# Optimization experiments

Measured on AMD Instinct MI355X. Metric: run time of the kernel, lower is better.

## Reference

```python
import jax, jax.numpy as jnp
import numpy as np

HIDDEN = 1024


def setup_inputs() -> dict:
    key = jax.random.key(0)
    ks = jax.random.split(key, 8)
    x_in, y_in, out_dim, hidden = 1024, 1024, 1024, HIDDEN
    Nx, Ny = 4096, 4096
    s = lambda d: 1.0 / np.sqrt(d)
    return {
        "x": jax.random.normal(ks[0], (Nx, x_in), jnp.float32),
        "y": jax.random.normal(ks[1], (Ny, y_in), jnp.float32),
        "Wq": jax.random.normal(ks[2], (hidden, x_in), jnp.float32) * s(x_in),
        "bq": jnp.zeros((hidden,), jnp.float32),
        "Wk": jax.random.normal(ks[3], (hidden, y_in), jnp.float32) * s(y_in),
        "bk": jnp.zeros((hidden,), jnp.float32),
        "Wv": jax.random.normal(ks[4], (out_dim, y_in), jnp.float32) * s(y_in),
        "bv": jnp.zeros((out_dim,), jnp.float32),
    }


def reference(x, y, Wq, bq, Wk, bk, Wv, bv):
    # Linear projections (torch Linear: x @ W.T + b)
    q = x @ Wq.T + bq          # [Nx, H]
    k = y @ Wk.T + bk          # [Ny, H]
    v = y @ Wv.T + bv          # [Ny, D_out]
    scores = (q @ k.T) / jnp.sqrt(jnp.asarray(HIDDEN, q.dtype))  # [Nx, Ny]
    attn = jax.nn.softmax(scores, axis=1)
    return attn @ v            # [Nx, D_out]
```

## Files before the change

kernel.cpp:

```cpp
#include <hip/hip_runtime.h>
#include <cstdint>
#include <cstddef>

typedef __attribute__((ext_vector_type(8))) __bf16 bf16x8;
typedef __attribute__((ext_vector_type(4))) float  f32x4;

#define WAITCNT_VM(n)   ((n & 0xF) | 0x70 | 0xF00 | (((n) >> 4) << 14))
#define WAITCNT_LGKM(n) (0xF | 0x70 | ((n) << 8) | (3 << 14))

__device__ __forceinline__ unsigned short f32_to_bf16(float f) {
    union { float f; unsigned int u; } cv;
    cv.f = f;
    unsigned int u = cv.u;
    return (unsigned short)((u + 0x7fffu + ((u >> 16) & 1u)) >> 16);
}

__device__ __forceinline__ float bf16_to_f32(unsigned short h) {
    union { unsigned int u; float f; } cv;
    cv.u = ((unsigned int)h) << 16;
    return cv.f;
}

__device__ __forceinline__ void async_copy16(const unsigned short* g, unsigned short* lds) {
    __builtin_amdgcn_global_load_lds(
        (const __attribute__((address_space(1))) unsigned int*)g,
        (__attribute__((address_space(3))) unsigned int*)lds,
        16, 0, 0);
}

__global__ __launch_bounds__(256) void cast_all(
    const float* __restrict__ x,  const float* __restrict__ y,
    const float* __restrict__ wq, const float* __restrict__ wk, const float* __restrict__ wv,
    unsigned short* __restrict__ xb,  unsigned short* __restrict__ yb,
    unsigned short* __restrict__ wqb, unsigned short* __restrict__ wkb,
    unsigned short* __restrict__ wvb, float* __restrict__ lsum)
{
    int b = blockIdx.x;
    if (b >= 11264) {
        float4 z = {0.f, 0.f, 0.f, 0.f};
#pragma unroll
        for (int t = 0; t < 4; ++t)
            ((float4*)lsum)[threadIdx.x * 4 + t] = z;
        return;
    }
    const float* s; unsigned short* d; int base;
    if      (b < 4096)  { s = x;  d = xb;  base = b; }
    else if (b < 8192)  { s = y;  d = yb;  base = b - 4096; }
    else if (b < 9216)  { s = wq; d = wqb; base = b - 8192; }
    else if (b < 10240) { s = wk; d = wkb; base = b - 9216; }
    else                { s = wv; d = wvb; base = b - 10240; }
    int i = base * 256 + threadIdx.x;
    float4 v = ((const float4*)s)[i];
    ushort4 o;
    o.x = f32_to_bf16(v.x);
    o.y = f32_to_bf16(v.y);
    o.z = f32_to_bf16(v.z);
    o.w = f32_to_bf16(v.w);
    ((ushort4*)d)[i] = o;
}

__device__ __forceinline__ void gemm_core_pf(
    const unsigned short* __restrict__ A, const unsigned short* __restrict__ B,
    int K, int rowBase, int colBase, int kBeg, int kEnd,
    unsigned short* ldsA, unsigned short* ldsB, f32x4 acc[4][4])
{
    const int tid  = threadIdx.x;
    const int lane = tid & 63;
    const int wave = tid >> 6;
    const int quad = lane >> 4;
    const int r    = lane & 15;
    const int wm   = wave >> 1;
    const int wn   = wave & 1;

    const int c1 = tid + 256;
    const long aOff0 = (long)(rowBase + (tid >> 2)) * K + (tid & 3) * 8;
    const long aOff1 = (long)(rowBase + (c1  >> 2)) * K + (c1  & 3) * 8;
    const long bOff0 = (long)(colBase + (tid >> 2)) * K + (tid & 3) * 8;
    const long bOff1 = (long)(colBase + (c1  >> 2)) * K + (c1  & 3) * 8;
    unsigned short* ldsA0 = ldsA + tid * 8;
    unsigned short* ldsA1 = ldsA + c1 * 8;
    unsigned short* ldsB0 = ldsB + tid * 8;
    unsigned short* ldsB1 = ldsB + c1 * 8;

    const int aReadOff = (wm * 64 + r) * 32 + quad * 8;
    const int bReadOff = (wn * 64 + r) * 32 + quad * 8;

    const int nSteps = (kEnd - kBeg) >> 5;

    async_copy16(A + aOff0 + kBeg, ldsA0);
    async_copy16(A + aOff1 + kBeg, ldsA1);
    async_copy16(B + bOff0 + kBeg, ldsB0);
    async_copy16(B + bOff1 + kBeg, ldsB1);

    for (int s = 0; s < nSteps; ++s) {
        const int cur = (s & 1) << 12;
        const int nxt = cur ^ 4096;
        __builtin_amdgcn_s_waitcnt(0);
        __syncthreads();
        if (s + 1 < nSteps) {
            const int kn = kBeg + ((s + 1) << 5);
            async_copy16(A + aOff0 + kn, ldsA0 + nxt);
            async_copy16(A + aOff1 + kn, ldsA1 + nxt);
            async_copy16(B + bOff0 + kn, ldsB0 + nxt);
            async_copy16(B + bOff1 + kn, ldsB1 + nxt);
        }
        bf16x8 af[4], bfr[4];
#pragma unroll
        for (int i = 0; i < 4; ++i)
            af[i] = *(const bf16x8*)(ldsA + cur + aReadOff + i * 16 * 32);
#pragma unroll
        for (int j = 0; j < 4; ++j)
            bfr[j] = *(const bf16x8*)(ldsB + cur + bReadOff + j * 16 * 32);
#pragma unroll
        for (int i = 0; i < 4; ++i)
#pragma unroll
            for (int j = 0; j < 4; ++j)
                acc[i][j] = __builtin_amdgcn_mfma_f32_16x16x32_bf16(af[i], bfr[j], acc[i][j], 0, 0, 0);
    }
}

__global__ __launch_bounds__(256, 2)
void proj_batched(const unsigned short* __restrict__ xb, const unsigned short* __restrict__ yb,
                  const unsigned short* __restrict__ wqb, const unsigned short* __restrict__ wkb,
                  const unsigned short* __restrict__ wvb,
                  unsigned short* __restrict__ q, unsigned short* __restrict__ k,
                  unsigned short* __restrict__ vt,
                  const float* __restrict__ bq, const float* __restrict__ bk,
                  const float* __restrict__ bv)
{
    __shared__ __align__(16) unsigned short ldsA[2 * 128 * 32];
    __shared__ __align__(16) unsigned short ldsB[2 * 128 * 32];

    const int b = blockIdx.x;
    const int z = b >> 8;
    const int rb = b & 255;

    const unsigned short *A, *B;
    unsigned short* C;
    const float* bias;
    int N, rowBase, colBase;
    bool biasPerRow;
    if (z == 0) {
        A = xb; B = wqb; C = q; bias = bq; N = 1024; biasPerRow = false;
        colBase = (rb >> 5) * 128; rowBase = (rb & 31) * 128;
    } else if (z == 1) {
        A = yb; B = wkb; C = k; bias = bk; N = 1024; biasPerRow = false;
        colBase = (rb >> 5) * 128; rowBase = (rb & 31) * 128;
    } else {
        A = wvb; B = yb; C = vt; bias = bv; N = 4096; biasPerRow = true;
        colBase = (rb >> 3) * 128; rowBase = (rb & 7) * 128;
    }

    f32x4 acc[4][4];
#pragma unroll
    for (int i = 0; i < 4; ++i)
#pragma unroll
        for (int j = 0; j < 4; ++j)
            acc[i][j] = (f32x4){0.f, 0.f, 0.f, 0.f};

    gemm_core_pf(A, B, 1024, rowBase, colBase, 0, 1024, ldsA, ldsB, acc);

    const int lane = threadIdx.x & 63;
    const int wave = threadIdx.x >> 6;
    const int quad = lane >> 4;
    const int r    = lane & 15;
    const int orow0 = rowBase + (wave >> 1) * 64 + quad * 4;
    const int ocol0 = colBase + (wave & 1) * 64 + r;

#pragma unroll
    for (int i = 0; i < 4; ++i)
#pragma unroll
        for (int e = 0; e < 4; ++e) {
            const int row = orow0 + i * 16 + e;
            const float brow = biasPerRow ? bias[row] : 0.f;
#pragma unroll
            for (int j = 0; j < 4; ++j) {
                const int col = ocol0 + j * 16;
                const float bb = biasPerRow ? brow : bias[col];
                C[(long)row * N + col] = f32_to_bf16(acc[i][j][e] + bb);
            }
        }
}

__device__ __forceinline__ void stage_half(const unsigned short* src, long rstep,
                                           unsigned short* ldsLane) {
    async_copy16(src, ldsLane);
    async_copy16(src + rstep, ldsLane + 4096);
}

__device__ __forceinline__ void gemm256_core(
    const unsigned short* __restrict__ A, const unsigned short* __restrict__ B,
    int K, int rowBase, int colBase, int kBeg, int nTiles,
    unsigned short* lds, f32x4 acc[8][4])
{
    const int tid  = threadIdx.x;
    const int lane = tid & 63;
    const int wid  = tid >> 6;
    const int quad = lane >> 4;
    const int r    = lane & 15;
    const int wm   = wid >> 2;
    const int wn   = wid & 3;

    const int row0 = tid >> 3;
    const int chs8 = (((tid & 7) ^ (row0 & 7)) << 3);
    const unsigned short* As = A + (long)(rowBase + row0) * K + chs8 + kBeg;
    const unsigned short* Bs = B + (long)(colBase + row0) * K + chs8 + kBeg;
    const long rstep = (long)K * 64;
    const long hstep = (long)K * 128;
    unsigned short* ldsLane = lds + tid * 8;

    const int aRd = (wm << 13) + (r << 6);
    const int bRd = 16384 + (wn << 12) + (r << 6);
    const int sw0 = ((quad ^ (r & 7)) << 3);
    const int sw1 = (((quad + 4) ^ (r & 7)) << 3);

    stage_half(As,         rstep, ldsLane);
    stage_half(As + hstep, rstep, ldsLane + 8192);
    stage_half(Bs,         rstep, ldsLane + 16384);
    stage_half(Bs + hstep, rstep, ldsLane + 24576);
    if (nTiles > 1) {
        stage_half(Bs + 64,         rstep, ldsLane + 32768 + 16384);
        stage_half(Bs + hstep + 64, rstep, ldsLane + 32768 + 24576);
    }
    __builtin_amdgcn_s_waitcnt(WAITCNT_VM(4));
    __builtin_amdgcn_s_barrier();
    __builtin_amdgcn_sched_barrier(0);

    bf16x8 aE[4], aO[4], bX[4], bY[4];
#pragma unroll
    for (int i = 0; i < 4; ++i)
        aE[i] = *(const bf16x8*)(lds + aRd + i * 1024 + sw0);
#pragma unroll
    for (int j = 0; j < 4; ++j)
        bX[j] = *(const bf16x8*)(lds + bRd + j * 1024 + sw0);

    for (int T = 0; T < nTiles; ++T) {
        const int cur = (T & 1) << 15;
        const int nxt = cur ^ 32768;

#pragma unroll
        for (int i = 0; i < 4; ++i)
            aO[i] = *(const bf16x8*)(lds + cur + aRd + (4 + i) * 1024 + sw0);
        __builtin_amdgcn_s_waitcnt(WAITCNT_LGKM(4));
        __builtin_amdgcn_sched_barrier(0);
        __builtin_amdgcn_s_setprio(1);
#pragma unroll
        for (int i = 0; i < 4; ++i)
#pragma unroll
            for (int j = 0; j < 4; ++j)
                acc[i][j] = __builtin_amdgcn_mfma_f32_16x16x32_bf16(aE[i], bX[j], acc[i][j], 0, 0, 0);
        __builtin_amdgcn_s_setprio(0);
        __builtin_amdgcn_sched_barrier(0);
        __builtin_amdgcn_s_barrier();
        if (T + 1 < nTiles) stage_half(As + (T + 1) * 64, rstep, ldsLane + nxt);

#pragma unroll
        for (int i = 0; i < 4; ++i)
            aE[i] = *(const bf16x8*)(lds + cur + aRd + i * 1024 + sw1);
#pragma unroll
        for (int j = 0; j < 4; ++j)
            bY[j] = *(const bf16x8*)(lds + cur + bRd + j * 1024 + sw1);
        __builtin_amdgcn_s_waitcnt(WAITCNT_LGKM(8));
        __builtin_amdgcn_sched_barrier(0);
        __builtin_amdgcn_s_setprio(1);
#pragma unroll
        for (int i = 0; i < 4; ++i)
#pragma unroll
            for (int j = 0; j < 4; ++j)
                acc[4 + i][j] = __builtin_amdgcn_mfma_f32_16x16x32_bf16(aO[i], bX[j], acc[4 + i][j], 0, 0, 0);
        __builtin_amdgcn_s_setprio(0);
        __builtin_amdgcn_sched_barrier(0);
        __builtin_amdgcn_s_barrier();
        if (T + 1 < nTiles) stage_half(As + hstep + (T + 1) * 64, rstep, ldsLane + nxt + 8192);

#pragma unroll
        for (int i = 0; i < 4; ++i)
            aO[i] = *(const bf16x8*)(lds + cur + aRd + (4 + i) * 1024 + sw1);
        __builtin_amdgcn_s_waitcnt(WAITCNT_LGKM(4));
        __builtin_amdgcn_sched_barrier(0);
        __builtin_amdgcn_s_setprio(1);
#pragma unroll
        for (int i = 0; i < 4; ++i)
#pragma unroll
            for (int j = 0; j < 4; ++j)
                acc[i][j] = __builtin_amdgcn_mfma_f32_16x16x32_bf16(aE[i], bY[j], acc[i][j], 0, 0, 0);
        __builtin_amdgcn_s_setprio(0);
        __builtin_amdgcn_sched_barrier(0);
        __builtin_amdgcn_s_barrier();
        if (T + 2 < nTiles) stage_half(Bs + (T + 2) * 64, rstep, ldsLane + cur + 16384);

        if (T + 1 < nTiles) {
            if (T + 2 < nTiles) __builtin_amdgcn_s_waitcnt(WAITCNT_VM(2));
            else                __builtin_amdgcn_s_waitcnt(WAITCNT_VM(0));
            __builtin_amdgcn_s_barrier();
            __builtin_amdgcn_sched_barrier(0);
#pragma unroll
            for (int i = 0; i < 4; ++i)
                aE[i] = *(const bf16x8*)(lds + nxt + aRd + i * 1024 + sw0);
#pragma unroll
            for (int j = 0; j < 4; ++j)
                bX[j] = *(const bf16x8*)(lds + nxt + bRd + j * 1024 + sw0);
            __builtin_amdgcn_s_waitcnt(WAITCNT_LGKM(8));
        } else {
            __builtin_amdgcn_s_waitcnt(WAITCNT_LGKM(0));
        }
        __builtin_amdgcn_sched_barrier(0);
        __builtin_amdgcn_s_setprio(1);
#pragma unroll
        for (int i = 0; i < 4; ++i)
#pragma unroll
            for (int j = 0; j < 4; ++j)
                acc[4 + i][j] = __builtin_amdgcn_mfma_f32_16x16x32_bf16(aO[i], bY[j], acc[4 + i][j], 0, 0, 0);
        __builtin_amdgcn_s_setprio(0);
        __builtin_amdgcn_sched_barrier(0);
        if (T + 2 < nTiles) stage_half(Bs + hstep + (T + 2) * 64, rstep, ldsLane + cur + 24576);
    }
}

__global__ __launch_bounds__(512, 2)
void scores_gemm256(const unsigned short* __restrict__ q, const unsigned short* __restrict__ k,
                    unsigned short* __restrict__ P, float* __restrict__ lsum, float scale2)
{
    __shared__ __align__(16) unsigned short lds[2 * 32768];

    const int bid = blockIdx.x;
    const int swz = (bid & 7) * 32 + (bid >> 3);
    const int mt = swz >> 4, nt = swz & 15;
    const int rowBase = mt * 256;
    const int colBase = nt * 256;

    f32x4 acc[8][4];
#pragma unroll
    for (int i = 0; i < 8; ++i)
#pragma unroll
        for (int j = 0; j < 4; ++j)
            acc[i][j] = (f32x4){0.f, 0.f, 0.f, 0.f};

    gemm256_core(q, k, 1024, rowBase, colBase, 0, 16, lds, acc);

    const int lane = threadIdx.x & 63;
    const int wid  = threadIdx.x >> 6;
    const int quad = lane >> 4;
    const int r    = lane & 15;
    const int orow0 = rowBase + (wid >> 2) * 128 + quad * 4;
    const int ocol0 = colBase + (wid & 3) * 64 + r;

#pragma unroll
    for (int mi = 0; mi < 8; ++mi)
#pragma unroll
        for (int e = 0; e < 4; ++e) {
            const int row = orow0 + mi * 16 + e;
            float rs = 0.f;
#pragma unroll
            for (int nj = 0; nj < 4; ++nj) {
                const float p = exp2f(acc[mi][nj][e] * scale2);
                rs += p;
                P[(long)row * 4096 + ocol0 + nj * 16] = f32_to_bf16(p);
            }
#pragma unroll
            for (int m = 1; m < 16; m <<= 1) rs += __shfl_xor(rs, m, 64);
            if (r == 0) atomicAdd(&lsum[row], rs);
        }
}

template <int ATOMIC>
__global__ __launch_bounds__(512, 2)
void out_gemm256(const unsigned short* __restrict__ P, const unsigned short* __restrict__ vt,
                 void* __restrict__ Out)
{
    __shared__ __align__(16) unsigned short lds[2 * 32768];

    const int bid = blockIdx.x;
    const int swz = (bid & 7) * 32 + (bid >> 3);
    const int z  = swz & 3;
    const int nt = (swz >> 2) & 3;
    const int mt = swz >> 4;
    const int rowBase = mt * 256;
    const int colBase = nt * 256;
    const int kBeg = z * 1024;

    f32x4 acc[8][4];
#pragma unroll
    for (int i = 0; i < 8; ++i)
#pragma unroll
        for (int j = 0; j < 4; ++j)
            acc[i][j] = (f32x4){0.f, 0.f, 0.f, 0.f};

    gemm256_core(P, vt, 4096, rowBase, colBase, kBeg, 16, lds, acc);

    const int lane = threadIdx.x & 63;
    const int wid  = threadIdx.x >> 6;
    const int quad = lane >> 4;
    const int r    = lane & 15;
    const int orow0 = rowBase + (wid >> 2) * 128 + quad * 4;
    const int ocol0 = colBase + (wid & 3) * 64 + r;

#pragma unroll
    for (int mi = 0; mi < 8; ++mi)
#pragma unroll
        for (int e = 0; e < 4; ++e) {
            const int row = orow0 + mi * 16 + e;
#pragma unroll
            for (int nj = 0; nj < 4; ++nj) {
                const int col = ocol0 + nj * 16;
                if (ATOMIC) {
                    atomicAdd(&((float*)Out)[(long)row * 1024 + col], acc[mi][nj][e]);
                } else {
                    unsigned short* parts = (unsigned short*)Out + (size_t)z * (4096 * 1024);
                    parts[(long)row * 1024 + col] = f32_to_bf16(acc[mi][nj][e]);
                }
            }
        }
}

__global__ __launch_bounds__(256) void reduce_norm4(const unsigned short* __restrict__ parts,
                                                    const float* __restrict__ lsum,
                                                    float* __restrict__ O) {
    const int i = blockIdx.x * 256 + threadIdx.x;
    const float inv = 1.0f / lsum[i >> 8];
    const size_t stride = (size_t)(4096 * 1024) / 4;
    ushort4 a = ((const ushort4*)parts)[i];
    ushort4 b = ((const ushort4*)parts)[i + stride];
    ushort4 c = ((const ushort4*)parts)[i + 2 * stride];
    ushort4 d = ((const ushort4*)parts)[i + 3 * stride];
    float4 o;
    o.x = (bf16_to_f32(a.x) + bf16_to_f32(b.x) + bf16_to_f32(c.x) + bf16_to_f32(d.x)) * inv;
    o.y = (bf16_to_f32(a.y) + bf16_to_f32(b.y) + bf16_to_f32(c.y) + bf16_to_f32(d.y)) * inv;
    o.z = (bf16_to_f32(a.z) + bf16_to_f32(b.z) + bf16_to_f32(c.z) + bf16_to_f32(d.z)) * inv;
    o.w = (bf16_to_f32(a.w) + bf16_to_f32(b.w) + bf16_to_f32(c.w) + bf16_to_f32(d.w)) * inv;
    ((float4*)O)[i] = o;
}

__global__ __launch_bounds__(256) void norm_rows(float* __restrict__ O, const float* __restrict__ lsum) {
    int i = blockIdx.x * 256 + threadIdx.x;
    const float inv = 1.0f / lsum[i >> 8];
    float4 v = ((const float4*)O)[i];
    v.x *= inv; v.y *= inv; v.z *= inv; v.w *= inv;
    ((float4*)O)[i] = v;
}

extern "C" void kernel_launch(void* const* d_in, const int* in_sizes, int n_in,
                              void* d_out, int out_size, void* d_ws, size_t ws_size,
                              hipStream_t stream) {
    const float* x  = (const float*)d_in[0];
    const float* y  = (const float*)d_in[1];
    const float* Wq = (const float*)d_in[2];
    const float* bq = (const float*)d_in[3];
    const float* Wk = (const float*)d_in[4];
    const float* bk = (const float*)d_in[5];
    const float* Wv = (const float*)d_in[6];
    const float* bv = (const float*)d_in[7];

    constexpr int Nx = 4096, Ny = 4096, H = 1024, Dv = 1024, Kin = 1024;

    char* ws = (char*)d_ws;
    size_t off = 0;
    auto carve = [&](size_t bytes) {
        char* p = ws + off;
        off += (bytes + 255) & ~(size_t)255;
        return p;
    };

    unsigned short* q_bf  = (unsigned short*)carve((size_t)Nx * H * 2);
    unsigned short* k_bf  = (unsigned short*)carve((size_t)Ny * H * 2);
    unsigned short* vt_bf = (unsigned short*)carve((size_t)Dv * Ny * 2);
    float*          lsum  = (float*)carve((size_t)Nx * sizeof(float));

    char* overlay = ws + off;
    unsigned short* x_bf  = (unsigned short*)overlay;
    unsigned short* y_bf  = x_bf  + (size_t)Nx * Kin;
    unsigned short* Wq_bf = y_bf  + (size_t)Ny * Kin;
    unsigned short* Wk_bf = Wq_bf + (size_t)H  * Kin;
    unsigned short* Wv_bf = Wk_bf + (size_t)H  * Kin;
    unsigned short* P_bf  = (unsigned short*)overlay;

    const size_t overlay_bytes = (size_t)Nx * Ny * 2;
    const size_t partsBytes = (size_t)Nx * Dv * 2;
    unsigned short* parts = (unsigned short*)(overlay + overlay_bytes);
    const size_t need_parts = (size_t)((overlay + overlay_bytes + 4 * partsBytes) - ws);
    const bool useParts = ws_size >= need_parts;

    if (!useParts)
        hipMemsetAsync(d_out, 0, (size_t)Nx * Dv * sizeof(float), stream);

    cast_all<<<11265, 256, 0, stream>>>(x, y, Wq, Wk, Wv, x_bf, y_bf, Wq_bf, Wk_bf, Wv_bf, lsum);

    proj_batched<<<768, 256, 0, stream>>>(x_bf, y_bf, Wq_bf, Wk_bf, Wv_bf,
                                          q_bf, k_bf, vt_bf, bq, bk, bv);

    const float scale2 = 1.4426950408889634f / 32.0f;
    scores_gemm256<<<256, 512, 0, stream>>>(q_bf, k_bf, P_bf, lsum, scale2);

    if (useParts) {
        out_gemm256<0><<<256, 512, 0, stream>>>(P_bf, vt_bf, parts);
        reduce_norm4<<<(Nx * Dv / 4) / 256, 256, 0, stream>>>(parts, lsum, (float*)d_out);
    } else {
        out_gemm256<1><<<256, 512, 0, stream>>>(P_bf, vt_bf, d_out);
        norm_rows<<<Nx * Dv / 4 / 256, 256, 0, stream>>>((float*)d_out, lsum);
    }
}
```

Measured before the change: 223.1 us.

## Prefetch A and B two tiles ahead and drop manual LDS waitcnts in GEMM loop

Reworks the double-buffered main loop of the 256x256 scores GEMM so both A and B tiles are prefetched two K-steps ahead, staged in pairs after barriers, instead of staging A one step ahead mid-iteration. It removes the explicit LGKM waitcnts and most sched_barriers, leaving the compiler to place LDS waits, and adds unroll 2 on the tile loop. This cuts intra-iteration barriers and gives global loads more time to land. In exchange the compiler's scheduling is less constrained, which may interleave MFMAs and LDS reads less well and raise register pressure.

```diff
diff --git a/kernel.cpp b/kernel.cpp
--- a/kernel.cpp
+++ b/kernel.cpp
@@ -6,7 +6,6 @@
 typedef __attribute__((ext_vector_type(4))) float  f32x4;
 
 #define WAITCNT_VM(n)   ((n & 0xF) | 0x70 | 0xF00 | (((n) >> 4) << 14))
-#define WAITCNT_LGKM(n) (0xF | 0x70 | ((n) << 8) | (3 << 14))
 
 __device__ __forceinline__ unsigned short f32_to_bf16(float f) {
     union { float f; unsigned int u; } cv;
@@ -219,10 +218,14 @@
     stage_half(Bs,         rstep, ldsLane + 16384);
     stage_half(Bs + hstep, rstep, ldsLane + 24576);
     if (nTiles > 1) {
-        stage_half(Bs + 64,         rstep, ldsLane + 32768 + 16384);
-        stage_half(Bs + hstep + 64, rstep, ldsLane + 32768 + 24576);
-    }
-    __builtin_amdgcn_s_waitcnt(WAITCNT_VM(4));
+        stage_half(As + 64,         rstep, ldsLane + 32768);
+        stage_half(As + hstep + 64, rstep, ldsLane + 40960);
+        stage_half(Bs + 64,         rstep, ldsLane + 49152);
+        stage_half(Bs + hstep + 64, rstep, ldsLane + 57344);
+        __builtin_amdgcn_s_waitcnt(WAITCNT_VM(8));
+    } else {
+        __builtin_amdgcn_s_waitcnt(WAITCNT_VM(0));
+    }
     __builtin_amdgcn_s_barrier();
     __builtin_amdgcn_sched_barrier(0);
 
@@ -234,6 +237,7 @@
     for (int j = 0; j < 4; ++j)
         bX[j] = *(const bf16x8*)(lds + bRd + j * 1024 + sw0);
 
+#pragma unroll 2
     for (int T = 0; T < nTiles; ++T) {
         const int cur = (T & 1) << 15;
         const int nxt = cur ^ 32768;
@@ -241,8 +245,6 @@
 #pragma unroll
         for (int i = 0; i < 4; ++i)
             aO[i] = *(const bf16x8*)(lds + cur + aRd + (4 + i) * 1024 + sw0);
-        __builtin_amdgcn_s_waitcnt(WAITCNT_LGKM(4));
-        __builtin_amdgcn_sched_barrier(0);
         __builtin_amdgcn_s_setprio(1);
 #pragma unroll
         for (int i = 0; i < 4; ++i)
@@ -250,9 +252,6 @@
             for (int j = 0; j < 4; ++j)
                 acc[i][j] = __builtin_amdgcn_mfma_f32_16x16x32_bf16(aE[i], bX[j], acc[i][j], 0, 0, 0);
         __builtin_amdgcn_s_setprio(0);
-        __builtin_amdgcn_sched_barrier(0);
-        __builtin_amdgcn_s_barrier();
-        if (T + 1 < nTiles) stage_half(As + (T + 1) * 64, rstep, ldsLane + nxt);
 
 #pragma unroll
         for (int i = 0; i < 4; ++i)
@@ -260,8 +259,6 @@
 #pragma unroll
         for (int j = 0; j < 4; ++j)
             bY[j] = *(const bf16x8*)(lds + cur + bRd + j * 1024 + sw1);
-        __builtin_amdgcn_s_waitcnt(WAITCNT_LGKM(8));
-        __builtin_amdgcn_sched_barrier(0);
         __builtin_amdgcn_s_setprio(1);
 #pragma unroll
         for (int i = 0; i < 4; ++i)
@@ -269,15 +266,10 @@
             for (int j = 0; j < 4; ++j)
                 acc[4 + i][j] = __builtin_amdgcn_mfma_f32_16x16x32_bf16(aO[i], bX[j], acc[4 + i][j], 0, 0, 0);
         __builtin_amdgcn_s_setprio(0);
-        __builtin_amdgcn_sched_barrier(0);
-        __builtin_amdgcn_s_barrier();
-        if (T + 1 < nTiles) stage_half(As + hstep + (T + 1) * 64, rstep, ldsLane + nxt + 8192);
 
 #pragma unroll
         for (int i = 0; i < 4; ++i)
             aO[i] = *(const bf16x8*)(lds + cur + aRd + (4 + i) * 1024 + sw1);
-        __builtin_amdgcn_s_waitcnt(WAITCNT_LGKM(4));
-        __builtin_amdgcn_sched_barrier(0);
         __builtin_amdgcn_s_setprio(1);
 #pragma unroll
         for (int i = 0; i < 4; ++i)
@@ -285,12 +277,14 @@
             for (int j = 0; j < 4; ++j)
                 acc[i][j] = __builtin_amdgcn_mfma_f32_16x16x32_bf16(aE[i], bY[j], acc[i][j], 0, 0, 0);
         __builtin_amdgcn_s_setprio(0);
-        __builtin_amdgcn_sched_barrier(0);
         __builtin_amdgcn_s_barrier();
-        if (T + 2 < nTiles) stage_half(Bs + (T + 2) * 64, rstep, ldsLane + cur + 16384);
+        if (T + 2 < nTiles) {
+            stage_half(Bs + (T + 2) * 64,         rstep, ldsLane + cur + 16384);
+            stage_half(Bs + hstep + (T + 2) * 64, rstep, ldsLane + cur + 24576);
+        }
 
         if (T + 1 < nTiles) {
-            if (T + 2 < nTiles) __builtin_amdgcn_s_waitcnt(WAITCNT_VM(2));
+            if (T + 2 < nTiles) __builtin_amdgcn_s_waitcnt(WAITCNT_VM(4));
             else                __builtin_amdgcn_s_waitcnt(WAITCNT_VM(0));
             __builtin_amdgcn_s_barrier();
             __builtin_amdgcn_sched_barrier(0);
@@ -300,11 +294,7 @@
 #pragma unroll
             for (int j = 0; j < 4; ++j)
                 bX[j] = *(const bf16x8*)(lds + nxt + bRd + j * 1024 + sw0);
-            __builtin_amdgcn_s_waitcnt(WAITCNT_LGKM(8));
-        } else {
-            __builtin_amdgcn_s_waitcnt(WAITCNT_LGKM(0));
-        }
-        __builtin_amdgcn_sched_barrier(0);
+        }
         __builtin_amdgcn_s_setprio(1);
 #pragma unroll
         for (int i = 0; i < 4; ++i)
@@ -312,8 +302,11 @@
             for (int j = 0; j < 4; ++j)
                 acc[4 + i][j] = __builtin_amdgcn_mfma_f32_16x16x32_bf16(aO[i], bY[j], acc[4 + i][j], 0, 0, 0);
         __builtin_amdgcn_s_setprio(0);
-        __builtin_amdgcn_sched_barrier(0);
-        if (T + 2 < nTiles) stage_half(Bs + hstep + (T + 2) * 64, rstep, ldsLane + cur + 24576);
+        __builtin_amdgcn_s_barrier();
+        if (T + 2 < nTiles) {
+            stage_half(As + (T + 2) * 64,         rstep, ldsLane + cur);
+            stage_half(As + hstep + (T + 2) * 64, rstep, ldsLane + cur + 8192);
+        }
     }
 }
 
```

Result: slower. 311.7 us (+39.7%).

## Add staggered ping-pong GEMM pipeline for the scores kernel

Applied to the files above, without the earlier changes.

Adds a new 256x256 GEMM core for the QK^T scores kernel in which the two halves of the workgroup (wm==0 vs wm==1) are offset in phase. One half issues its LDS reads before its first MFMA block, the other after, so that LDS traffic and matrix-core work from different waves overlap. The MFMA schedule is regrouped into four 4x2 sub-blocks, and the A and B prefetch order changes: A is staged two tiles ahead and B one tile ahead. The PV kernel keeps the old core under a new name. Risks include barrier and waitcnt correctness under the new staging order and higher register pressure from the larger fragment arrays.

```diff
diff --git a/kernel.cpp b/kernel.cpp
--- a/kernel.cpp
+++ b/kernel.cpp
@@ -182,13 +182,26 @@
         }
 }
 
-__device__ __forceinline__ void stage_half(const unsigned short* src, long rstep,
-                                           unsigned short* ldsLane) {
-    async_copy16(src, ldsLane);
-    async_copy16(src + rstep, ldsLane + 4096);
-}
-
-__device__ __forceinline__ void gemm256_core(
+#define G256_RD_A(arr, bufOff, mo) \
+    { _Pragma("unroll") for (int m = 0; m < 4; ++m) { \
+        arr[m]     = *(const bf16x8*)(lds + (bufOff) + aRd + ((mo) + m) * 1024 + sw0); \
+        arr[4 + m] = *(const bf16x8*)(lds + (bufOff) + aRd + ((mo) + m) * 1024 + sw1); } }
+#define G256_RD_B(arr, bufOff, no) \
+    { _Pragma("unroll") for (int n = 0; n < 2; ++n) { \
+        arr[n]     = *(const bf16x8*)(lds + (bufOff) + bRd + ((no) + n) * 1024 + sw0); \
+        arr[2 + n] = *(const bf16x8*)(lds + (bufOff) + bRd + ((no) + n) * 1024 + sw1); } }
+#define G256_MFMA(mb, nb, Af, Bf) \
+    { _Pragma("unroll") for (int kq = 0; kq < 2; ++kq) \
+      _Pragma("unroll") for (int m = 0; m < 4; ++m) \
+      _Pragma("unroll") for (int n = 0; n < 2; ++n) \
+        acc[(mb) + m][(nb) + n] = __builtin_amdgcn_mfma_f32_16x16x32_bf16( \
+            Af[kq * 4 + m], Bf[kq * 2 + n], acc[(mb) + m][(nb) + n], 0, 0, 0); }
+#define G256_BAR  __builtin_amdgcn_s_barrier()
+#define G256_SB   __builtin_amdgcn_sched_barrier(0)
+#define G256_PR1  __builtin_amdgcn_s_setprio(1)
+#define G256_PR0  __builtin_amdgcn_s_setprio(0)
+
+__device__ __forceinline__ void gemm256_la(
     const unsigned short* __restrict__ A, const unsigned short* __restrict__ B,
     int K, int rowBase, int colBase, int kBeg, int nTiles,
     unsigned short* lds, f32x4 acc[8][4])
@@ -214,17 +227,22 @@
     const int sw0 = ((quad ^ (r & 7)) << 3);
     const int sw1 = (((quad + 4) ^ (r & 7)) << 3);
 
-    stage_half(As,         rstep, ldsLane);
-    stage_half(As + hstep, rstep, ldsLane + 8192);
-    stage_half(Bs,         rstep, ldsLane + 16384);
-    stage_half(Bs + hstep, rstep, ldsLane + 24576);
+    auto STG = [&](const unsigned short* src, int ldsOff) {
+        async_copy16(src,         ldsLane + ldsOff);
+        async_copy16(src + rstep, ldsLane + ldsOff + 4096);
+    };
+
+    STG(As,         0);
+    STG(As + hstep, 8192);
+    STG(Bs,         16384);
+    STG(Bs + hstep, 24576);
     if (nTiles > 1) {
-        stage_half(Bs + 64,         rstep, ldsLane + 32768 + 16384);
-        stage_half(Bs + hstep + 64, rstep, ldsLane + 32768 + 24576);
+        STG(Bs + 64,         32768 + 16384);
+        STG(Bs + hstep + 64, 32768 + 24576);
     }
     __builtin_amdgcn_s_waitcnt(WAITCNT_VM(4));
-    __builtin_amdgcn_s_barrier();
-    __builtin_amdgcn_sched_barrier(0);
+    G256_BAR;
+    G256_SB;
 
     bf16x8 aE[4], aO[4], bX[4], bY[4];
 #pragma unroll
@@ -242,17 +260,17 @@
         for (int i = 0; i < 4; ++i)
             aO[i] = *(const bf16x8*)(lds + cur + aRd + (4 + i) * 1024 + sw0);
         __builtin_amdgcn_s_waitcnt(WAITCNT_LGKM(4));
-        __builtin_amdgcn_sched_barrier(0);
-        __builtin_amdgcn_s_setprio(1);
+        G256_SB;
+        G256_PR1;
 #pragma unroll
         for (int i = 0; i < 4; ++i)
 #pragma unroll
             for (int j = 0; j < 4; ++j)
                 acc[i][j] = __builtin_amdgcn_mfma_f32_16x16x32_bf16(aE[i], bX[j], acc[i][j], 0, 0, 0);
-        __builtin_amdgcn_s_setprio(0);
-        __builtin_amdgcn_sched_barrier(0);
-        __builtin_amdgcn_s_barrier();
-        if (T + 1 < nTiles) stage_half(As + (T + 1) * 64, rstep, ldsLane + nxt);
+        G256_PR0;
+        G256_SB;
+        G256_BAR;
+        if (T + 1 < nTiles) STG(As + (T + 1) * 64, nxt);
 
 #pragma unroll
         for (int i = 0; i < 4; ++i)
@@ -261,39 +279,39 @@
         for (int j = 0; j < 4; ++j)
             bY[j] = *(const bf16x8*)(lds + cur + bRd + j * 1024 + sw1);
         __builtin_amdgcn_s_waitcnt(WAITCNT_LGKM(8));
-        __builtin_amdgcn_sched_barrier(0);
-        __builtin_amdgcn_s_setprio(1);
+        G256_SB;
+        G256_PR1;
 #pragma unroll
         for (int i = 0; i < 4; ++i)
 #pragma unroll
             for (int j = 0; j < 4; ++j)
                 acc[4 + i][j] = __builtin_amdgcn_mfma_f32_16x16x32_bf16(aO[i], bX[j], acc[4 + i][j], 0, 0, 0);
-        __builtin_amdgcn_s_setprio(0);
-        __builtin_amdgcn_sched_barrier(0);
-        __builtin_amdgcn_s_barrier();
-        if (T + 1 < nTiles) stage_half(As + hstep + (T + 1) * 64, rstep, ldsLane + nxt + 8192);
+        G256_PR0;
+        G256_SB;
+        G256_BAR;
+        if (T + 1 < nTiles) STG(As + hstep + (T + 1) * 64, nxt + 8192);
 
 #pragma unroll
         for (int i = 0; i < 4; ++i)
             aO[i] = *(const bf16x8*)(lds + cur + aRd + (4 + i) * 1024 + sw1);
         __builtin_amdgcn_s_waitcnt(WAITCNT_LGKM(4));
-        __builtin_amdgcn_sched_barrier(0);
-        __builtin_amdgcn_s_setprio(1);
+        G256_SB;
+        G256_PR1;
 #pragma unroll
         for (int i = 0; i < 4; ++i)
 #pragma unroll
             for (int j = 0; j < 4; ++j)
                 acc[i][j] = __builtin_amdgcn_mfma_f32_16x16x32_bf16(aE[i], bY[j], acc[i][j], 0, 0, 0);
-        __builtin_amdgcn_s_setprio(0);
-        __builtin_amdgcn_sched_barrier(0);
-        __builtin_amdgcn_s_barrier();
-        if (T + 2 < nTiles) stage_half(Bs + (T + 2) * 64, rstep, ldsLane + cur + 16384);
+        G256_PR0;
+        G256_SB;
+        G256_BAR;
+        if (T + 2 < nTiles) STG(Bs + (T + 2) * 64, cur + 16384);
 
         if (T + 1 < nTiles) {
             if (T + 2 < nTiles) __builtin_amdgcn_s_waitcnt(WAITCNT_VM(2));
             else                __builtin_amdgcn_s_waitcnt(WAITCNT_VM(0));
-            __builtin_amdgcn_s_barrier();
-            __builtin_amdgcn_sched_barrier(0);
+            G256_BAR;
+            G256_SB;
 #pragma unroll
             for (int i = 0; i < 4; ++i)
                 aE[i] = *(const bf16x8*)(lds + nxt + aRd + i * 1024 + sw0);
@@ -304,17 +322,117 @@
         } else {
             __builtin_amdgcn_s_waitcnt(WAITCNT_LGKM(0));
         }
-        __builtin_amdgcn_sched_barrier(0);
-        __builtin_amdgcn_s_setprio(1);
+        G256_SB;
+        G256_PR1;
 #pragma unroll
         for (int i = 0; i < 4; ++i)
 #pragma unroll
             for (int j = 0; j < 4; ++j)
                 acc[4 + i][j] = __builtin_amdgcn_mfma_f32_16x16x32_bf16(aO[i], bY[j], acc[4 + i][j], 0, 0, 0);
-        __builtin_amdgcn_s_setprio(0);
-        __builtin_amdgcn_sched_barrier(0);
-        if (T + 2 < nTiles) stage_half(Bs + hstep + (T + 2) * 64, rstep, ldsLane + cur + 24576);
-    }
+        G256_PR0;
+        G256_SB;
+        if (T + 2 < nTiles) STG(Bs + hstep + (T + 2) * 64, cur + 24576);
+    }
+}
+
+__device__ __forceinline__ void gemm256_stag(
+    const unsigned short* __restrict__ A, const unsigned short* __restrict__ B,
+    int K, int rowBase, int colBase, int kBeg, int nTiles,
+    unsigned short* lds, f32x4 acc[8][4])
+{
+    const int tid  = threadIdx.x;
+    const int lane = tid & 63;
+    const int wid  = tid >> 6;
+    const int quad = lane >> 4;
+    const int r    = lane & 15;
+    const int wm   = wid >> 2;
+    const int wn   = wid & 3;
+
+    const int row0 = tid >> 3;
+    const int chs8 = (((tid & 7) ^ (row0 & 7)) << 3);
+    const unsigned short* As = A + (long)(rowBase + row0) * K + chs8 + kBeg;
+    const unsigned short* Bs = B + (long)(colBase + row0) * K + chs8 + kBeg;
+    const long rstep = (long)K * 64;
+    const long hstep = (long)K * 128;
+    unsigned short* ldsLane = lds + tid * 8;
+
+    auto STG = [&](const unsigned short* src, int ldsOff) {
+        async_copy16(src,         ldsLane + ldsOff);
+        async_copy16(src + rstep, ldsLane + ldsOff + 4096);
+    };
+
+    const int aRd = (wm << 13) + (r << 6);
+    const int bRd = 16384 + (wn << 12) + (r << 6);
+    const int sw0 = ((quad ^ (r & 7)) << 3);
+    const int sw1 = (((quad + 4) ^ (r & 7)) << 3);
+
+    STG(As,         0);
+    STG(As + hstep, 8192);
+    STG(Bs,         16384);
+    STG(Bs + hstep, 24576);
+    if (nTiles > 1) {
+        STG(As + 64,         32768);
+        STG(As + 64 + hstep, 40960);
+    }
+    __builtin_amdgcn_s_waitcnt(WAITCNT_VM(4));
+    G256_BAR;
+    G256_SB;
+
+    bf16x8 aLo[8], aHi[8], bLo[4], bHi[4];
+    G256_RD_A(aLo, 0, 0); G256_RD_B(bLo, 0, 0);
+
+    for (int t = 0; t < nTiles; ++t) {
+        const int cur = (t & 1) << 15;
+        const int nxt = cur ^ 32768;
+        const bool s1 = t + 1 < nTiles, s2 = t + 2 < nTiles;
+
+        if (wm == 0) {
+            G256_RD_A(aHi, cur, 4); G256_RD_B(bHi, cur, 2);
+            __builtin_amdgcn_s_waitcnt(WAITCNT_LGKM(12));
+            G256_SB;
+            G256_PR1; G256_MFMA(0, 0, aLo, bLo); G256_PR0;
+            if (s1) STG(Bs + (t + 1) * 64, nxt + 16384);
+            __builtin_amdgcn_s_waitcnt(WAITCNT_LGKM(0));
+            G256_SB;
+            G256_PR1; G256_MFMA(4, 0, aHi, bLo); G256_PR0;
+            if (s1) STG(Bs + hstep + (t + 1) * 64, nxt + 24576);
+            G256_PR1; G256_MFMA(4, 2, aHi, bHi); G256_PR0;
+            G256_BAR;
+            G256_SB;
+            G256_PR1; G256_MFMA(0, 2, aLo, bHi); G256_PR0;
+            if (s2) {
+                STG(As + (t + 2) * 64,         cur);
+                STG(As + hstep + (t + 2) * 64, cur + 8192);
+            }
+        } else {
+            __builtin_amdgcn_s_waitcnt(WAITCNT_LGKM(0));
+            G256_SB;
+            G256_PR1; G256_MFMA(0, 0, aLo, bLo); G256_PR0;
+            G256_RD_A(aHi, cur, 4); G256_RD_B(bHi, cur, 2);
+            if (s1) STG(Bs + (t + 1) * 64, nxt + 16384);
+            __builtin_amdgcn_s_waitcnt(WAITCNT_LGKM(0));
+            G256_SB;
+            G256_PR1; G256_MFMA(4, 0, aHi, bLo); G256_PR0;
+            if (s1) STG(Bs + hstep + (t + 1) * 64, nxt + 24576);
+            G256_PR1; G256_MFMA(4, 2, aHi, bHi); G256_PR0;
+            G256_BAR;
+            G256_SB;
+            G256_PR1; G256_MFMA(0, 2, aLo, bHi); G256_PR0;
+            if (s2) {
+                STG(As + (t + 2) * 64,         cur);
+                STG(As + hstep + (t + 2) * 64, cur + 8192);
+            }
+        }
+
+        if (s1) {
+            if (s2) __builtin_amdgcn_s_waitcnt(WAITCNT_VM(4));
+            else    __builtin_amdgcn_s_waitcnt(WAITCNT_VM(0));
+            G256_BAR;
+            G256_SB;
+            G256_RD_A(aLo, nxt, 0); G256_RD_B(bLo, nxt, 0);
+        }
+    }
+    __builtin_amdgcn_s_waitcnt(WAITCNT_LGKM(0));
 }
 
 __global__ __launch_bounds__(512, 2)
@@ -336,7 +454,7 @@
         for (int j = 0; j < 4; ++j)
             acc[i][j] = (f32x4){0.f, 0.f, 0.f, 0.f};
 
-    gemm256_core(q, k, 1024, rowBase, colBase, 0, 16, lds, acc);
+    gemm256_stag(q, k, 1024, rowBase, colBase, 0, 16, lds, acc);
 
     const int lane = threadIdx.x & 63;
     const int wid  = threadIdx.x >> 6;
@@ -386,7 +504,7 @@
         for (int j = 0; j < 4; ++j)
             acc[i][j] = (f32x4){0.f, 0.f, 0.f, 0.f};
 
-    gemm256_core(P, vt, 4096, rowBase, colBase, kBeg, 16, lds, acc);
+    gemm256_la(P, vt, 4096, rowBase, colBase, kBeg, 16, lds, acc);
 
     const int lane = threadIdx.x & 63;
     const int wid  = threadIdx.x >> 6;
```

Measured after the change: 233.3 us. 4.6% more time.
